# Performance work log

Measured on AMD Instinct MI355X. Metric: run time of the kernel, lower is better.

The kernel has to match this reference:

```python
import jax, jax.numpy as jnp
from jax import lax
import numpy as np

N_ATOMS, N_BONDS, N_GRAPHS = 8192, 32768, 256
EMBED, HIDDEN, DEPTH = 32, 256, 10
ATOM_VOCAB, BOND_VOCAB = 200, 10


def setup_inputs() -> dict:
    key = jax.random.key(0)
    ks = jax.random.split(key, 16)
    f = lambda k, *sh: jax.random.normal(k, sh, dtype=jnp.float32) * 0.05
    return {
        "atom_features": jax.random.randint(ks[0], (N_ATOMS,), 0, ATOM_VOCAB),
        "bond_features": jax.random.randint(ks[1], (N_BONDS,), 0, BOND_VOCAB),
        "adjacency_matrix": jax.random.randint(ks[2], (N_ATOMS, N_ATOMS), 0, 2, dtype=jnp.int32),
        "batch_indices": jax.random.randint(ks[3], (N_ATOMS,), 0, N_GRAPHS),
        "atom_emb": f(ks[4], ATOM_VOCAB, EMBED),
        "bond_emb": f(ks[5], BOND_VOCAB, EMBED),
        "msg_W": f(ks[6], DEPTH, HIDDEN, 2 * EMBED),
        "msg_b": f(ks[7], DEPTH, HIDDEN),
        "gru_Wih": f(ks[8], DEPTH, 3 * EMBED, HIDDEN),
        "gru_Whh": f(ks[9], DEPTH, 3 * EMBED, EMBED),
        "gru_bih": f(ks[10], DEPTH, 3 * EMBED),
        "gru_bhh": f(ks[11], DEPTH, 3 * EMBED),
        "pool_W": f(ks[12], HIDDEN, EMBED),
        "pool_b": f(ks[13], HIDDEN),
    }


def _gmpn(atom_emb, bond_emb, msg_W, msg_b, gru_Wih, gru_Whh, gru_bih, gru_bhh,
          pool_W, pool_b, atom_features, bond_features, adjacency_matrix, batch_indices):
    H = atom_emb[atom_features]                       # [N, E]
    A = (adjacency_matrix > 0).astype(H.dtype)        # [N, N] 0/1
    deg = A.sum(axis=1)                               # [N]
    has_nb = deg > 0
    inv_deg = jnp.where(has_nb, 1.0 / jnp.maximum(deg, 1.0), 0.0)[:, None]

    def layer(h, params):
        W, b, wih, whh, b_ih, b_hh = params
        # mean_j Linear([h_i ; h_j]) = W1 h_i + W2 mean_j h_j + b
        neigh_mean = (A @ h) * inv_deg                # [N, E]
        W1, W2 = W[:, :EMBED], W[:, EMBED:]
        msg = h @ W1.T + neigh_mean @ W2.T + b        # [N, HIDDEN]
        msg = jnp.where(has_nb[:, None], msg, 0.0)    # zero message if no neighbors
        # single-step GRU: input=msg, hidden state=h
        gi = msg @ wih.T + b_ih
        gh = h @ whh.T + b_hh
        ir, iz, inn = jnp.split(gi, 3, axis=-1)
        hr, hz, hn = jnp.split(gh, 3, axis=-1)
        r = jax.nn.sigmoid(ir + hr)
        z = jax.nn.sigmoid(iz + hz)
        n = jnp.tanh(inn + r * hn)
        h_new = (1.0 - z) * n + z * h                 # [N, E]
        return h_new, None

    H, _ = lax.scan(layer, H, (msg_W, msg_b, gru_Wih, gru_Whh, gru_bih, gru_bhh))

    # per-graph mean pooling (zeros for empty graphs), then global_pool linear
    seg_sum = jax.ops.segment_sum(H, batch_indices, num_segments=N_GRAPHS)
    cnt = jax.ops.segment_sum(jnp.ones((H.shape[0],), H.dtype), batch_indices, num_segments=N_GRAPHS)
    graph_mean = jnp.where(cnt[:, None] > 0, seg_sum / jnp.maximum(cnt, 1.0)[:, None], 0.0)
    graph_embeddings = graph_mean @ pool_W.T + pool_b  # [G, HIDDEN]

    bond_embeddings = bond_emb[bond_features]          # [B, E]
    return H, bond_embeddings, graph_embeddings


def reference(atom_features, bond_features, adjacency_matrix, batch_indices,
              atom_emb, bond_emb, msg_W, msg_b, gru_Wih, gru_Whh, gru_bih, gru_bhh,
              pool_W, pool_b):
    return _gmpn(atom_emb, bond_emb, msg_W, msg_b, gru_Wih, gru_Whh, gru_bih, gru_bhh,
                 pool_W, pool_b, atom_features, bond_features, adjacency_matrix, batch_indices)
```

## Files before the change

kernel.cpp:

```cpp
#include <hip/hip_runtime.h>
#include <stdint.h>

typedef __bf16 bf16x8 __attribute__((ext_vector_type(8)));
typedef float f32x4 __attribute__((ext_vector_type(4)));

__device__ __forceinline__ float b2f(unsigned short u){
  unsigned int t = ((unsigned int)u) << 16;
  return __builtin_bit_cast(float, t);
}
__device__ __forceinline__ unsigned short f2b(float f){
  unsigned int x = __builtin_bit_cast(unsigned int, f);
  x = x + 0x7FFFu + ((x >> 16) & 1u);
  return (unsigned short)(x >> 16);
}
__device__ __forceinline__ void spread8(unsigned int B, unsigned int w[4]){
  unsigned int m = __umul24(B, 0x8001u);
  w[0] = __umul24(m & 0x00010001u, 0x3F80u);
  w[1] = __umul24(m & 0x00040004u, 0x0FE0u);
  w[2] = __umul24(m & 0x00100010u, 0x03F8u);
  w[3] = __umul24(m & 0x00400040u, 0x00FEu);
}
__device__ __forceinline__ float fsig(float x){ return 1.f/(1.f + __expf(-x)); }
__device__ __forceinline__ float ftanh(float x){ return 1.f - 2.f/(__expf(2.f*x) + 1.f); }

__global__ void k_prep(const void* s_msgW, const void* s_msgb, const void* s_wih,
                       const void* s_whh, const void* s_bih, const void* s_bhh,
                       const void* s_poolW, const void* s_poolb,
                       const unsigned short* __restrict__ aemb_u16,
                       unsigned short* __restrict__ cw,
                       int* __restrict__ deg, float* __restrict__ seg,
                       float* __restrict__ cnt, int* __restrict__ flag){
  int b = blockIdx.x, t = threadIdx.x;
  unsigned int uu = aemb_u16[2*t];
  int e = (int)((uu >> 7) & 0xFF);
  unsigned long long vote = __ballot(e >= 100 && e <= 127);
  int isb = (__popcll(vote) > 32) ? 1 : 0;
  if (b < 1771){
    int id = b*256 + t;
    if (id < 453248){
      const void* src; int off;
      if      (id < 163840){ src = s_msgW;  off = id; }
      else if (id < 166400){ src = s_msgb;  off = id - 163840; }
      else if (id < 412160){ src = s_wih;   off = id - 166400; }
      else if (id < 442880){ src = s_whh;   off = id - 412160; }
      else if (id < 443840){ src = s_bih;   off = id - 442880; }
      else if (id < 444800){ src = s_bhh;   off = id - 443840; }
      else if (id < 452992){ src = s_poolW; off = id - 444800; }
      else                 { src = s_poolb; off = id - 452992; }
      cw[id] = isb ? ((const unsigned short*)src)[off]
                   : f2b(((const float*)src)[off]);
    }
  } else {
    int id2 = (b - 1771)*256 + t;
    if (id2 < 8192){ deg[id2] = 0; seg[id2] = 0.f; }
    if (id2 < 256) cnt[id2] = 0.f;
    if (b == 1771 && t == 0) flag[0] = isb;
  }
}

__global__ void k_pack(const int* __restrict__ adj, unsigned int* __restrict__ mask3,
                       int* __restrict__ deg){
  int tid = blockIdx.x*256 + threadIdx.x;
  int rb  = tid >> 12;
  int rem = tid & 4095;
  int kgg = rem >> 6;
  int L   = rem & 63;
  int lc = L & 15, q = L >> 4;
  int row = rb*16 + lc;
  const int* arow = adj + (size_t)row*8192 + kgg*128 + q*8;
  unsigned int dw = 0; int pc = 0;
  #pragma unroll
  for (int s=0;s<4;s++){
    const int* p = arow + s*32;
    unsigned int b = 0;
    #pragma unroll
    for (int t=0;t<8;t++) b |= (p[t] > 0 ? 1u : 0u) << t;
    dw |= b << (8*s);
    pc += __popc(b);
  }
  mask3[tid] = dw;
  pc += __shfl_xor(pc, 16);
  pc += __shfl_xor(pc, 32);
  if (q == 0) atomicAdd(deg + row, pc);
}

__global__ void k_bond(const int* __restrict__ bft, const void* __restrict__ braw,
                       const int* __restrict__ flag,
                       unsigned short* __restrict__ outB16, float* __restrict__ outB32){
  int id = blockIdx.x*256 + threadIdx.x;
  int e = id >> 5, c = id & 31;
  int idx = bft[e]*32 + c;
  if (flag[0]) outB16[id] = ((const unsigned short*)braw)[idx];
  else         outB32[id] = ((const float*)braw)[idx];
}

__global__ void k_embed(const int* __restrict__ af, const void* __restrict__ araw,
                        const int* __restrict__ flag,
                        float* __restrict__ hf32, uint4* __restrict__ hfrag){
  __shared__ __align__(16) float sh[512];
  int t = threadIdx.x;
  int r = t >> 5, c = t & 31;
  int row = blockIdx.x*16 + r;
  int idx = af[row]*32 + c;
  float f;
  if (flag[0]) f = b2f(((const unsigned short*)araw)[idx]);
  else         f = ((const float*)araw)[idx];
  hf32[row*32 + c] = f;
  sh[r*32 + c] = f;
  __syncthreads();
  if (t < 64){
    int nt = t >> 5, Lq = t & 31;
    int ks32 = blockIdx.x >> 1, half = blockIdx.x & 1;
    int col = nt*16 + (Lq & 15);
    int rbase = (Lq >> 4)*8;
    unsigned int w[4];
    #pragma unroll
    for (int p=0;p<4;p++){
      unsigned int lo = f2b(sh[(rbase + 2*p    )*32 + col]);
      unsigned int hi = f2b(sh[(rbase + 2*p + 1)*32 + col]);
      w[p] = lo | (hi << 16);
    }
    hfrag[(ks32*2 + nt)*64 + half*32 + Lq] = make_uint4(w[0],w[1],w[2],w[3]);
  }
}

__launch_bounds__(512)
__global__ void k_layer(const unsigned int* __restrict__ mask3,
                        const uint4* __restrict__ hfragIn,
                        unsigned int* __restrict__ hfragOut,
                        float* __restrict__ hf32,
                        const int* __restrict__ deg,
                        const unsigned short* __restrict__ msgW,
                        const unsigned short* __restrict__ msgb,
                        const unsigned short* __restrict__ wih,
                        const unsigned short* __restrict__ whh,
                        const unsigned short* __restrict__ bih,
                        const unsigned short* __restrict__ bhh,
                        const int* __restrict__ bidx,
                        float* __restrict__ seg, float* __restrict__ cnt,
                        unsigned short* __restrict__ out16, float* __restrict__ out32,
                        const int* __restrict__ flag, int last)
{
  __shared__ __align__(16) char uni[33792];
  __shared__ __align__(16) unsigned short sA[32][72];
  __shared__ __align__(16) unsigned short smsg[32][264];
  __shared__ int sdeg[32];

  const int t = threadIdx.x;
  const int b = blockIdx.x;
  const int w = t >> 6, L = t & 63;
  const int q = L >> 4, lc = L & 15;
  const int rowbase = b*32;

  const int r0 = t >> 4;
  const int cl = t & 15;
  const int r  = rowbase + r0;
  const int isb = flag[0];
  const int dgr = deg[r];
  const float invr = dgr > 0 ? 1.f/(float)dgr : 0.f;
  float h0 = hf32[r*32 + cl];
  float h1 = hf32[r*32 + 16 + cl];
  sA[r0][cl]    = f2b(h0);
  sA[r0][16+cl] = f2b(h1);
  if (cl == 0) sdeg[r0] = dgr;

  {
    f32x4 a00={0,0,0,0}, a01={0,0,0,0}, a10={0,0,0,0}, a11={0,0,0,0};
    const unsigned int* mp = mask3 + (size_t)b*8192 + w*512 + L;
    const uint4* bp = hfragIn + (size_t)w*4096 + L;
    for (int g=0; g<8; g++){
      unsigned int mw0 = mp[g*64];
      unsigned int mw1 = mp[4096 + g*64];
      #pragma unroll
      for (int s=0; s<4; s++){
        int ks = g*4 + s;
        uint4 u0 = bp[ks*128];
        uint4 u1 = bp[ks*128 + 64];
        union { unsigned int u[4]; bf16x8 v; } A0, A1, B0, B1;
        spread8((mw0 >> (8*s)) & 0xFFu, A0.u);
        spread8((mw1 >> (8*s)) & 0xFFu, A1.u);
        B0.u[0]=u0.x; B0.u[1]=u0.y; B0.u[2]=u0.z; B0.u[3]=u0.w;
        B1.u[0]=u1.x; B1.u[1]=u1.y; B1.u[2]=u1.z; B1.u[3]=u1.w;
        a00 = __builtin_amdgcn_mfma_f32_16x16x32_bf16(A0.v, B0.v, a00, 0,0,0);
        a01 = __builtin_amdgcn_mfma_f32_16x16x32_bf16(A0.v, B1.v, a01, 0,0,0);
        a10 = __builtin_amdgcn_mfma_f32_16x16x32_bf16(A1.v, B0.v, a10, 0,0,0);
        a11 = __builtin_amdgcn_mfma_f32_16x16x32_bf16(A1.v, B1.v, a11, 0,0,0);
      }
    }
    float* sp = (float*)uni + w*1056;
    #pragma unroll
    for (int rg=0; rg<4; rg++){
      int rw = q*4 + rg;
      sp[rw*33 + lc]         = a00[rg];
      sp[rw*33 + 16 + lc]    = a01[rg];
      sp[(16+rw)*33 + lc]    = a10[rg];
      sp[(16+rw)*33 + 16+lc] = a11[rg];
    }
  }
  __syncthreads();
  {
    const float* spf = (const float*)uni;
    float s0 = 0.f, s1 = 0.f;
    #pragma unroll
    for (int ww=0; ww<8; ww++){
      s0 += spf[ww*1056 + r0*33 + cl];
      s1 += spf[ww*1056 + r0*33 + 16 + cl];
    }
    sA[r0][32+cl] = f2b(s0*invr);
    sA[r0][48+cl] = f2b(s1*invr);
  }
  __syncthreads();
  {
    int rt = w & 1, ntb = (w >> 1)*4;
    union { uint4 u; bf16x8 v; } A0, A1;
    A0.u = *(const uint4*)&sA[rt*16 + lc][q*8];
    A1.u = *(const uint4*)&sA[rt*16 + lc][32 + q*8];
    #pragma unroll
    for (int i=0; i<4; i++){
      int nt = ntb + i;
      union { uint4 u; bf16x8 v; } B0, B1;
      B0.u = *(const uint4*)(msgW + (size_t)(nt*16 + lc)*64 + q*8);
      B1.u = *(const uint4*)(msgW + (size_t)(nt*16 + lc)*64 + 32 + q*8);
      f32x4 am = {0,0,0,0};
      am = __builtin_amdgcn_mfma_f32_16x16x32_bf16(A0.v, B0.v, am, 0,0,0);
      am = __builtin_amdgcn_mfma_f32_16x16x32_bf16(A1.v, B1.v, am, 0,0,0);
      float bv = b2f(msgb[nt*16 + lc]);
      #pragma unroll
      for (int rg=0; rg<4; rg++){
        int rw = rt*16 + q*4 + rg;
        float v = am[rg] + bv;
        if (sdeg[rw] == 0) v = 0.f;
        smsg[rw][nt*16 + lc] = f2b(v);
      }
    }
  }
  __syncthreads();
  {
    float* sgi = (float*)uni;
    float* sgh = (float*)(uni + 12800);
    if (w < 6){
      int nt = w;
      f32x4 g0 = {0,0,0,0}, g1 = {0,0,0,0};
      #pragma unroll
      for (int ks=0; ks<8; ks++){
        union { uint4 u; bf16x8 v; } A0, A1, B;
        B.u  = *(const uint4*)(wih + (size_t)(nt*16 + lc)*256 + ks*32 + q*8);
        A0.u = *(const uint4*)&smsg[lc][ks*32 + q*8];
        A1.u = *(const uint4*)&smsg[16 + lc][ks*32 + q*8];
        g0 = __builtin_amdgcn_mfma_f32_16x16x32_bf16(A0.v, B.v, g0, 0,0,0);
        g1 = __builtin_amdgcn_mfma_f32_16x16x32_bf16(A1.v, B.v, g1, 0,0,0);
      }
      #pragma unroll
      for (int rg=0; rg<4; rg++){
        sgi[(q*4+rg)*100      + nt*16 + lc] = g0[rg];
        sgi[(16+q*4+rg)*100   + nt*16 + lc] = g1[rg];
      }
    } else {
      int rt = w - 6;
      union { uint4 u; bf16x8 v; } A;
      A.u = *(const uint4*)&sA[rt*16 + lc][q*8];
      #pragma unroll
      for (int nt=0; nt<6; nt++){
        union { uint4 u; bf16x8 v; } B;
        B.u = *(const uint4*)(whh + (size_t)(nt*16 + lc)*32 + q*8);
        f32x4 hh = {0,0,0,0};
        hh = __builtin_amdgcn_mfma_f32_16x16x32_bf16(A.v, B.v, hh, 0,0,0);
        #pragma unroll
        for (int rg=0; rg<4; rg++)
          sgh[(rt*16 + q*4+rg)*100 + nt*16 + lc] = hh[rg];
      }
    }
  }
  __syncthreads();
  {
    const float* sgi = (const float*)uni;
    const float* sgh = (const float*)(uni + 12800);
    float ir0 = sgi[r0*100 + cl]    + b2f(bih[cl]),    hr0 = sgh[r0*100 + cl]    + b2f(bhh[cl]);
    float iz0 = sgi[r0*100 + 32+cl] + b2f(bih[32+cl]), hz0 = sgh[r0*100 + 32+cl] + b2f(bhh[32+cl]);
    float in0 = sgi[r0*100 + 64+cl] + b2f(bih[64+cl]), hn0 = sgh[r0*100 + 64+cl] + b2f(bhh[64+cl]);
    float ir1 = sgi[r0*100 + 16+cl] + b2f(bih[16+cl]), hr1 = sgh[r0*100 + 16+cl] + b2f(bhh[16+cl]);
    float iz1 = sgi[r0*100 + 48+cl] + b2f(bih[48+cl]), hz1 = sgh[r0*100 + 48+cl] + b2f(bhh[48+cl]);
    float in1 = sgi[r0*100 + 80+cl] + b2f(bih[80+cl]), hn1 = sgh[r0*100 + 80+cl] + b2f(bhh[80+cl]);
    float rr0 = fsig(ir0 + hr0), zz0 = fsig(iz0 + hz0);
    float rr1 = fsig(ir1 + hr1), zz1 = fsig(iz1 + hz1);
    float nn0 = ftanh(in0 + rr0*hn0);
    float nn1 = ftanh(in1 + rr1*hn1);
    h0 = (1.f - zz0)*nn0 + zz0*h0;
    h1 = (1.f - zz1)*nn1 + zz1*h1;
    hf32[r*32 + cl]      = h0;
    hf32[r*32 + 16 + cl] = h1;
    unsigned int m0 = f2b(h0), m1 = f2b(h1);
    unsigned int p0 = (unsigned int)__shfl_xor((int)m0, 16);
    unsigned int p1 = (unsigned int)__shfl_xor((int)m1, 16);
    if ((r & 1) == 0){
      int ks32 = r >> 5;
      int Lf = ((r >> 3) & 3)*16 + cl;
      int pidx = (r & 7) >> 1;
      hfragOut[((ks32*2 + 0)*64 + Lf)*4 + pidx] = m0 | (p0 << 16);
      hfragOut[((ks32*2 + 1)*64 + Lf)*4 + pidx] = m1 | (p1 << 16);
    }
    if (last){
      if (isb){ out16[r*32 + cl] = (unsigned short)m0; out16[r*32 + 16 + cl] = (unsigned short)m1; }
      else    { out32[r*32 + cl] = h0; out32[r*32 + 16 + cl] = h1; }
      int gb = bidx[r];
      atomicAdd(seg + gb*32 + cl, h0);
      atomicAdd(seg + gb*32 + 16 + cl, h1);
      if (cl == 0) atomicAdd(cnt + gb, 1.f);
    }
  }
}

__global__ void k_pool(const float* __restrict__ seg, const float* __restrict__ cnt,
                       const unsigned short* __restrict__ pw, const unsigned short* __restrict__ pb,
                       const int* __restrict__ flag,
                       unsigned short* __restrict__ outG16, float* __restrict__ outG32){
  int g = blockIdx.x, o = threadIdx.x;
  float cv = cnt[g];
  float ic = cv > 0.f ? 1.f/cv : 0.f;
  float s = 0.f;
  #pragma unroll
  for (int c=0;c<32;c++) s += seg[g*32+c]*ic*b2f(pw[o*32+c]);
  s += b2f(pb[o]);
  if (flag[0]) outG16[g*256 + o] = f2b(s);
  else         outG32[g*256 + o] = s;
}

extern "C" void kernel_launch(void* const* d_in, const int* in_sizes, int n_in,
                              void* d_out, int out_size, void* d_ws, size_t ws_size,
                              hipStream_t stream){
  const int* af   = (const int*)d_in[0];
  const int* bft  = (const int*)d_in[1];
  const int* adj  = (const int*)d_in[2];
  const int* bidx = (const int*)d_in[3];

  char* ws = (char*)d_ws;
  unsigned int*   mask3  = (unsigned int*)(ws + 0);
  unsigned int*   hfrag0 = (unsigned int*)(ws + 8388608);
  unsigned int*   hfrag1 = (unsigned int*)(ws + 8912896);
  float*          hf32   = (float*)(ws + 9437184);
  int*            deg    = (int*)(ws + 10485760);
  float*          seg    = (float*)(ws + 10518528);
  float*          cnt    = (float*)(ws + 10551296);
  int*            flag   = (int*)(ws + 10552320);
  unsigned short* cw     = (unsigned short*)(ws + 10552384);

  unsigned short* o16 = (unsigned short*)d_out;
  float*          o32 = (float*)d_out;

  k_prep<<<1803, 256, 0, stream>>>(d_in[6], d_in[7], d_in[8], d_in[9], d_in[10],
                                   d_in[11], d_in[12], d_in[13],
                                   (const unsigned short*)d_in[4],
                                   cw, deg, seg, cnt, flag);
  k_pack<<<8192, 256, 0, stream>>>(adj, mask3, deg);
  k_bond<<<4096, 256, 0, stream>>>(bft, d_in[5], flag, o16 + 262144, o32 + 262144);
  k_embed<<<512, 512, 0, stream>>>(af, d_in[4], flag, hf32, (uint4*)hfrag0);

  for (int d = 0; d < 10; d++){
    const uint4*  hin  = (const uint4*)((d & 1) ? hfrag1 : hfrag0);
    unsigned int* hout = (d & 1) ? hfrag0 : hfrag1;
    k_layer<<<256, 512, 0, stream>>>(mask3, hin, hout, hf32, deg,
                                     cw + (size_t)d*16384,        cw + 163840 + d*256,
                                     cw + 166400 + (size_t)d*24576, cw + 412160 + d*3072,
                                     cw + 442880 + d*96,          cw + 443840 + d*96,
                                     bidx, seg, cnt, o16, o32, flag, (d == 9) ? 1 : 0);
  }
  k_pool<<<256, 256, 0, stream>>>(seg, cnt, cw + 444800, cw + 452992, flag,
                                  o16 + 1310720, o32 + 1310720);
}
```

Before: 532.7 us.

## Halve layer tile to 16 rows, prefetch adjacency fragments, fold bond gather into prep

The per-layer kernel now processes 16 rows per block with 256 threads and 512 blocks, so more CUs are busy than with the previous 256 blocks. Each wave covers a longer K range. Its adjacency-times-h loop is software-pipelined with register double-buffering of the mask and B fragments. The bond embedding gather is merged into the prep kernel to remove one launch. In exchange, the weight loads are repeated across twice as many blocks, register pressure rises from the prefetch buffers, and each block now handles one row tile instead of two, so fragment reuse drops.

```diff
diff --git a/kernel.cpp b/kernel.cpp
--- a/kernel.cpp
+++ b/kernel.cpp
@@ -27,9 +27,11 @@
                        const void* s_whh, const void* s_bih, const void* s_bhh,
                        const void* s_poolW, const void* s_poolb,
                        const unsigned short* __restrict__ aemb_u16,
+                       const int* __restrict__ bft, const void* __restrict__ braw,
                        unsigned short* __restrict__ cw,
                        int* __restrict__ deg, float* __restrict__ seg,
-                       float* __restrict__ cnt, int* __restrict__ flag){
+                       float* __restrict__ cnt, int* __restrict__ flag,
+                       unsigned short* __restrict__ outB16, float* __restrict__ outB32){
   int b = blockIdx.x, t = threadIdx.x;
   unsigned int uu = aemb_u16[2*t];
   int e = (int)((uu >> 7) & 0xFF);
@@ -50,11 +52,17 @@
       cw[id] = isb ? ((const unsigned short*)src)[off]
                    : f2b(((const float*)src)[off]);
     }
-  } else {
+  } else if (b < 1804){
     int id2 = (b - 1771)*256 + t;
     if (id2 < 8192){ deg[id2] = 0; seg[id2] = 0.f; }
     if (id2 < 256) cnt[id2] = 0.f;
     if (b == 1771 && t == 0) flag[0] = isb;
+  } else {
+    int id = (b - 1804)*256 + t;
+    int e2 = id >> 5, c = id & 31;
+    int idx = bft[e2]*32 + c;
+    if (isb) outB16[id] = ((const unsigned short*)braw)[idx];
+    else     outB32[id] = ((const float*)braw)[idx];
   }
 }
 
@@ -84,16 +92,6 @@
   if (q == 0) atomicAdd(deg + row, pc);
 }
 
-__global__ void k_bond(const int* __restrict__ bft, const void* __restrict__ braw,
-                       const int* __restrict__ flag,
-                       unsigned short* __restrict__ outB16, float* __restrict__ outB32){
-  int id = blockIdx.x*256 + threadIdx.x;
-  int e = id >> 5, c = id & 31;
-  int idx = bft[e]*32 + c;
-  if (flag[0]) outB16[id] = ((const unsigned short*)braw)[idx];
-  else         outB32[id] = ((const float*)braw)[idx];
-}
-
 __global__ void k_embed(const int* __restrict__ af, const void* __restrict__ araw,
                         const int* __restrict__ flag,
                         float* __restrict__ hf32, uint4* __restrict__ hfrag){
@@ -124,7 +122,7 @@
   }
 }
 
-__launch_bounds__(512)
+__launch_bounds__(256, 2)
 __global__ void k_layer(const unsigned int* __restrict__ mask3,
                         const uint4* __restrict__ hfragIn,
                         unsigned int* __restrict__ hfragOut,
@@ -141,16 +139,16 @@
                         unsigned short* __restrict__ out16, float* __restrict__ out32,
                         const int* __restrict__ flag, int last)
 {
-  __shared__ __align__(16) char uni[33792];
-  __shared__ __align__(16) unsigned short sA[32][72];
-  __shared__ __align__(16) unsigned short smsg[32][264];
-  __shared__ int sdeg[32];
+  __shared__ __align__(16) float uni[3200];
+  __shared__ __align__(16) unsigned short sA[16][72];
+  __shared__ __align__(16) unsigned short smsg[16][264];
+  __shared__ int sdeg[16];
 
   const int t = threadIdx.x;
   const int b = blockIdx.x;
   const int w = t >> 6, L = t & 63;
   const int q = L >> 4, lc = L & 15;
-  const int rowbase = b*32;
+  const int rowbase = b*16;
 
   const int r0 = t >> 4;
   const int cl = t & 15;
@@ -165,59 +163,65 @@
   if (cl == 0) sdeg[r0] = dgr;
 
   {
-    f32x4 a00={0,0,0,0}, a01={0,0,0,0}, a10={0,0,0,0}, a11={0,0,0,0};
-    const unsigned int* mp = mask3 + (size_t)b*8192 + w*512 + L;
-    const uint4* bp = hfragIn + (size_t)w*4096 + L;
-    for (int g=0; g<8; g++){
-      unsigned int mw0 = mp[g*64];
-      unsigned int mw1 = mp[4096 + g*64];
+    f32x4 a0 = {0,0,0,0}, a1 = {0,0,0,0};
+    const unsigned int* mp = mask3 + (size_t)b*4096 + (size_t)w*1024 + L;
+    const uint4* bp = hfragIn + (size_t)w*8192 + L;
+    unsigned int mw = mp[0];
+    uint4 buf[8];
+    #pragma unroll
+    for (int u=0; u<8; u++) buf[u] = bp[u*64];
+    #pragma unroll
+    for (int g=0; g<16; g++){
+      unsigned int mw_n = 0;
+      uint4 nbuf[8];
+      if (g < 15){
+        mw_n = mp[(g+1)*64];
+        #pragma unroll
+        for (int u=0; u<8; u++) nbuf[u] = bp[(g+1)*512 + u*64];
+      }
       #pragma unroll
       for (int s=0; s<4; s++){
-        int ks = g*4 + s;
-        uint4 u0 = bp[ks*128];
-        uint4 u1 = bp[ks*128 + 64];
-        union { unsigned int u[4]; bf16x8 v; } A0, A1, B0, B1;
-        spread8((mw0 >> (8*s)) & 0xFFu, A0.u);
-        spread8((mw1 >> (8*s)) & 0xFFu, A1.u);
+        union { unsigned int u[4]; bf16x8 v; } A, B0, B1;
+        spread8((mw >> (8*s)) & 0xFFu, A.u);
+        uint4 u0 = buf[s*2], u1 = buf[s*2+1];
         B0.u[0]=u0.x; B0.u[1]=u0.y; B0.u[2]=u0.z; B0.u[3]=u0.w;
         B1.u[0]=u1.x; B1.u[1]=u1.y; B1.u[2]=u1.z; B1.u[3]=u1.w;
-        a00 = __builtin_amdgcn_mfma_f32_16x16x32_bf16(A0.v, B0.v, a00, 0,0,0);
-        a01 = __builtin_amdgcn_mfma_f32_16x16x32_bf16(A0.v, B1.v, a01, 0,0,0);
-        a10 = __builtin_amdgcn_mfma_f32_16x16x32_bf16(A1.v, B0.v, a10, 0,0,0);
-        a11 = __builtin_amdgcn_mfma_f32_16x16x32_bf16(A1.v, B1.v, a11, 0,0,0);
-      }
-    }
-    float* sp = (float*)uni + w*1056;
+        a0 = __builtin_amdgcn_mfma_f32_16x16x32_bf16(A.v, B0.v, a0, 0,0,0);
+        a1 = __builtin_amdgcn_mfma_f32_16x16x32_bf16(A.v, B1.v, a1, 0,0,0);
+      }
+      mw = mw_n;
+      if (g < 15){
+        #pragma unroll
+        for (int u=0; u<8; u++) buf[u] = nbuf[u];
+      }
+    }
+    float* sp = uni + w*528;
     #pragma unroll
     for (int rg=0; rg<4; rg++){
       int rw = q*4 + rg;
-      sp[rw*33 + lc]         = a00[rg];
-      sp[rw*33 + 16 + lc]    = a01[rg];
-      sp[(16+rw)*33 + lc]    = a10[rg];
-      sp[(16+rw)*33 + 16+lc] = a11[rg];
-    }
-  }
-  __syncthreads();
-  {
-    const float* spf = (const float*)uni;
+      sp[rw*33 + lc]      = a0[rg];
+      sp[rw*33 + 16 + lc] = a1[rg];
+    }
+  }
+  __syncthreads();
+  {
     float s0 = 0.f, s1 = 0.f;
     #pragma unroll
-    for (int ww=0; ww<8; ww++){
-      s0 += spf[ww*1056 + r0*33 + cl];
-      s1 += spf[ww*1056 + r0*33 + 16 + cl];
+    for (int ww=0; ww<4; ww++){
+      s0 += uni[ww*528 + r0*33 + cl];
+      s1 += uni[ww*528 + r0*33 + 16 + cl];
     }
     sA[r0][32+cl] = f2b(s0*invr);
     sA[r0][48+cl] = f2b(s1*invr);
   }
   __syncthreads();
   {
-    int rt = w & 1, ntb = (w >> 1)*4;
     union { uint4 u; bf16x8 v; } A0, A1;
-    A0.u = *(const uint4*)&sA[rt*16 + lc][q*8];
-    A1.u = *(const uint4*)&sA[rt*16 + lc][32 + q*8];
+    A0.u = *(const uint4*)&sA[lc][q*8];
+    A1.u = *(const uint4*)&sA[lc][32 + q*8];
     #pragma unroll
     for (int i=0; i<4; i++){
-      int nt = ntb + i;
+      int nt = w*4 + i;
       union { uint4 u; bf16x8 v; } B0, B1;
       B0.u = *(const uint4*)(msgW + (size_t)(nt*16 + lc)*64 + q*8);
       B1.u = *(const uint4*)(msgW + (size_t)(nt*16 + lc)*64 + 32 + q*8);
@@ -227,7 +231,7 @@
       float bv = b2f(msgb[nt*16 + lc]);
       #pragma unroll
       for (int rg=0; rg<4; rg++){
-        int rw = rt*16 + q*4 + rg;
+        int rw = q*4 + rg;
         float v = am[rg] + bv;
         if (sdeg[rw] == 0) v = 0.f;
         smsg[rw][nt*16 + lc] = f2b(v);
@@ -236,29 +240,28 @@
   }
   __syncthreads();
   {
-    float* sgi = (float*)uni;
-    float* sgh = (float*)(uni + 12800);
-    if (w < 6){
-      int nt = w;
+    float* sgi = uni;
+    float* sgh = uni + 1600;
+    if (w < 3){
+      int nt0 = w*2, nt1 = w*2 + 1;
       f32x4 g0 = {0,0,0,0}, g1 = {0,0,0,0};
       #pragma unroll
       for (int ks=0; ks<8; ks++){
-        union { uint4 u; bf16x8 v; } A0, A1, B;
-        B.u  = *(const uint4*)(wih + (size_t)(nt*16 + lc)*256 + ks*32 + q*8);
-        A0.u = *(const uint4*)&smsg[lc][ks*32 + q*8];
-        A1.u = *(const uint4*)&smsg[16 + lc][ks*32 + q*8];
-        g0 = __builtin_amdgcn_mfma_f32_16x16x32_bf16(A0.v, B.v, g0, 0,0,0);
-        g1 = __builtin_amdgcn_mfma_f32_16x16x32_bf16(A1.v, B.v, g1, 0,0,0);
+        union { uint4 u; bf16x8 v; } A, B0, B1;
+        A.u  = *(const uint4*)&smsg[lc][ks*32 + q*8];
+        B0.u = *(const uint4*)(wih + (size_t)(nt0*16 + lc)*256 + ks*32 + q*8);
+        B1.u = *(const uint4*)(wih + (size_t)(nt1*16 + lc)*256 + ks*32 + q*8);
+        g0 = __builtin_amdgcn_mfma_f32_16x16x32_bf16(A.v, B0.v, g0, 0,0,0);
+        g1 = __builtin_amdgcn_mfma_f32_16x16x32_bf16(A.v, B1.v, g1, 0,0,0);
       }
       #pragma unroll
       for (int rg=0; rg<4; rg++){
-        sgi[(q*4+rg)*100      + nt*16 + lc] = g0[rg];
-        sgi[(16+q*4+rg)*100   + nt*16 + lc] = g1[rg];
+        sgi[(q*4+rg)*100 + nt0*16 + lc] = g0[rg];
+        sgi[(q*4+rg)*100 + nt1*16 + lc] = g1[rg];
       }
     } else {
-      int rt = w - 6;
       union { uint4 u; bf16x8 v; } A;
-      A.u = *(const uint4*)&sA[rt*16 + lc][q*8];
+      A.u = *(const uint4*)&sA[lc][q*8];
       #pragma unroll
       for (int nt=0; nt<6; nt++){
         union { uint4 u; bf16x8 v; } B;
@@ -267,14 +270,14 @@
         hh = __builtin_amdgcn_mfma_f32_16x16x32_bf16(A.v, B.v, hh, 0,0,0);
         #pragma unroll
         for (int rg=0; rg<4; rg++)
-          sgh[(rt*16 + q*4+rg)*100 + nt*16 + lc] = hh[rg];
-      }
-    }
-  }
-  __syncthreads();
-  {
-    const float* sgi = (const float*)uni;
-    const float* sgh = (const float*)(uni + 12800);
+          sgh[(q*4+rg)*100 + nt*16 + lc] = hh[rg];
+      }
+    }
+  }
+  __syncthreads();
+  {
+    const float* sgi = uni;
+    const float* sgh = uni + 1600;
     float ir0 = sgi[r0*100 + cl]    + b2f(bih[cl]),    hr0 = sgh[r0*100 + cl]    + b2f(bhh[cl]);
     float iz0 = sgi[r0*100 + 32+cl] + b2f(bih[32+cl]), hz0 = sgh[r0*100 + 32+cl] + b2f(bhh[32+cl]);
     float in0 = sgi[r0*100 + 64+cl] + b2f(bih[64+cl]), hn0 = sgh[r0*100 + 64+cl] + b2f(bhh[64+cl]);
@@ -347,21 +350,22 @@
   unsigned short* o16 = (unsigned short*)d_out;
   float*          o32 = (float*)d_out;
 
-  k_prep<<<1803, 256, 0, stream>>>(d_in[6], d_in[7], d_in[8], d_in[9], d_in[10],
+  k_prep<<<5900, 256, 0, stream>>>(d_in[6], d_in[7], d_in[8], d_in[9], d_in[10],
                                    d_in[11], d_in[12], d_in[13],
                                    (const unsigned short*)d_in[4],
-                                   cw, deg, seg, cnt, flag);
+                                   bft, d_in[5],
+                                   cw, deg, seg, cnt, flag,
+                                   o16 + 262144, o32 + 262144);
   k_pack<<<8192, 256, 0, stream>>>(adj, mask3, deg);
-  k_bond<<<4096, 256, 0, stream>>>(bft, d_in[5], flag, o16 + 262144, o32 + 262144);
   k_embed<<<512, 512, 0, stream>>>(af, d_in[4], flag, hf32, (uint4*)hfrag0);
 
   for (int d = 0; d < 10; d++){
     const uint4*  hin  = (const uint4*)((d & 1) ? hfrag1 : hfrag0);
     unsigned int* hout = (d & 1) ? hfrag0 : hfrag1;
-    k_layer<<<256, 512, 0, stream>>>(mask3, hin, hout, hf32, deg,
-                                     cw + (size_t)d*16384,        cw + 163840 + d*256,
+    k_layer<<<512, 256, 0, stream>>>(mask3, hin, hout, hf32, deg,
+                                     cw + (size_t)d*16384,          cw + 163840 + d*256,
                                      cw + 166400 + (size_t)d*24576, cw + 412160 + d*3072,
-                                     cw + 442880 + d*96,          cw + 443840 + d*96,
+                                     cw + 442880 + d*96,            cw + 443840 + d*96,
                                      bidx, seg, cnt, o16, o32, flag, (d == 9) ? 1 : 0);
   }
   k_pool<<<256, 256, 0, stream>>>(seg, cnt, cw + 444800, cw + 452992, flag,
```

Measured after the change: 581.8 us. 9.2% more time.

## Fuse embed, all GRU layers and pooling into one cooperative persistent kernel

Applied to the files above, without the earlier changes.

Replaces the per-layer kernel launches, the embed kernel and the pool kernel with a single cooperative kernel of 256 blocks that keeps the hidden state in registers and uses a global atomic barrier between layers. The bond gather is folded into the prep kernel. This removes launch overhead and the fp32 hidden-state round trip through global memory, at the cost of spin-wait grid barriers and requiring all blocks to be co-resident.

```diff
diff --git a/kernel.cpp b/kernel.cpp
--- a/kernel.cpp
+++ b/kernel.cpp
@@ -23,13 +23,28 @@
 __device__ __forceinline__ float fsig(float x){ return 1.f/(1.f + __expf(-x)); }
 __device__ __forceinline__ float ftanh(float x){ return 1.f - 2.f/(__expf(2.f*x) + 1.f); }
 
+__device__ __forceinline__ void gbar(int* bar, int target){
+  __syncthreads();
+  if (threadIdx.x == 0){
+    __threadfence();
+    __hip_atomic_fetch_add(bar, 1, __ATOMIC_RELAXED, __HIP_MEMORY_SCOPE_AGENT);
+    while (__hip_atomic_load(bar, __ATOMIC_RELAXED, __HIP_MEMORY_SCOPE_AGENT) < target)
+      __builtin_amdgcn_s_sleep(1);
+    __threadfence();
+  }
+  __syncthreads();
+}
+
 __global__ void k_prep(const void* s_msgW, const void* s_msgb, const void* s_wih,
                        const void* s_whh, const void* s_bih, const void* s_bhh,
                        const void* s_poolW, const void* s_poolb,
                        const unsigned short* __restrict__ aemb_u16,
+                       const int* __restrict__ bft, const void* __restrict__ braw,
                        unsigned short* __restrict__ cw,
                        int* __restrict__ deg, float* __restrict__ seg,
-                       float* __restrict__ cnt, int* __restrict__ flag){
+                       float* __restrict__ cnt, int* __restrict__ flag,
+                       int* __restrict__ bar,
+                       unsigned short* __restrict__ outB16, float* __restrict__ outB32){
   int b = blockIdx.x, t = threadIdx.x;
   unsigned int uu = aemb_u16[2*t];
   int e = (int)((uu >> 7) & 0xFF);
@@ -50,11 +65,20 @@
       cw[id] = isb ? ((const unsigned short*)src)[off]
                    : f2b(((const float*)src)[off]);
     }
-  } else {
+  } else if (b < 1804){
     int id2 = (b - 1771)*256 + t;
     if (id2 < 8192){ deg[id2] = 0; seg[id2] = 0.f; }
     if (id2 < 256) cnt[id2] = 0.f;
-    if (b == 1771 && t == 0) flag[0] = isb;
+    if (b == 1771){
+      if (t < 16) bar[t] = 0;
+      if (t == 0) flag[0] = isb;
+    }
+  } else {
+    int id = (b - 1804)*256 + t;
+    int e2 = id >> 5, c = id & 31;
+    int idx = bft[e2]*32 + c;
+    if (isb) outB16[id] = ((const unsigned short*)braw)[idx];
+    else     outB32[id] = ((const float*)braw)[idx];
   }
 }
 
@@ -84,245 +108,215 @@
   if (q == 0) atomicAdd(deg + row, pc);
 }
 
-__global__ void k_bond(const int* __restrict__ bft, const void* __restrict__ braw,
-                       const int* __restrict__ flag,
-                       unsigned short* __restrict__ outB16, float* __restrict__ outB32){
-  int id = blockIdx.x*256 + threadIdx.x;
-  int e = id >> 5, c = id & 31;
-  int idx = bft[e]*32 + c;
-  if (flag[0]) outB16[id] = ((const unsigned short*)braw)[idx];
-  else         outB32[id] = ((const float*)braw)[idx];
-}
-
-__global__ void k_embed(const int* __restrict__ af, const void* __restrict__ araw,
-                        const int* __restrict__ flag,
-                        float* __restrict__ hf32, uint4* __restrict__ hfrag){
-  __shared__ __align__(16) float sh[512];
-  int t = threadIdx.x;
-  int r = t >> 5, c = t & 31;
-  int row = blockIdx.x*16 + r;
-  int idx = af[row]*32 + c;
-  float f;
-  if (flag[0]) f = b2f(((const unsigned short*)araw)[idx]);
-  else         f = ((const float*)araw)[idx];
-  hf32[row*32 + c] = f;
-  sh[r*32 + c] = f;
-  __syncthreads();
-  if (t < 64){
-    int nt = t >> 5, Lq = t & 31;
-    int ks32 = blockIdx.x >> 1, half = blockIdx.x & 1;
-    int col = nt*16 + (Lq & 15);
-    int rbase = (Lq >> 4)*8;
-    unsigned int w[4];
-    #pragma unroll
-    for (int p=0;p<4;p++){
-      unsigned int lo = f2b(sh[(rbase + 2*p    )*32 + col]);
-      unsigned int hi = f2b(sh[(rbase + 2*p + 1)*32 + col]);
-      w[p] = lo | (hi << 16);
-    }
-    hfrag[(ks32*2 + nt)*64 + half*32 + Lq] = make_uint4(w[0],w[1],w[2],w[3]);
-  }
-}
-
-__launch_bounds__(512)
-__global__ void k_layer(const unsigned int* __restrict__ mask3,
-                        const uint4* __restrict__ hfragIn,
-                        unsigned int* __restrict__ hfragOut,
-                        float* __restrict__ hf32,
-                        const int* __restrict__ deg,
-                        const unsigned short* __restrict__ msgW,
-                        const unsigned short* __restrict__ msgb,
-                        const unsigned short* __restrict__ wih,
-                        const unsigned short* __restrict__ whh,
-                        const unsigned short* __restrict__ bih,
-                        const unsigned short* __restrict__ bhh,
-                        const int* __restrict__ bidx,
-                        float* __restrict__ seg, float* __restrict__ cnt,
-                        unsigned short* __restrict__ out16, float* __restrict__ out32,
-                        const int* __restrict__ flag, int last)
+__launch_bounds__(512, 1)
+__global__ void k_net(const int* __restrict__ af, const int* __restrict__ bidx,
+                      const void* __restrict__ aemb_raw, const int* __restrict__ flag,
+                      const unsigned int* __restrict__ mask3,
+                      unsigned int* __restrict__ hfrag0, unsigned int* __restrict__ hfrag1,
+                      const int* __restrict__ deg, const unsigned short* __restrict__ cw,
+                      unsigned short* __restrict__ out16, float* __restrict__ out32,
+                      float* __restrict__ seg, float* __restrict__ cnt, int* bar)
 {
-  __shared__ __align__(16) char uni[33792];
+  __shared__ __align__(16) float uni[8448];
   __shared__ __align__(16) unsigned short sA[32][72];
   __shared__ __align__(16) unsigned short smsg[32][264];
   __shared__ int sdeg[32];
 
-  const int t = threadIdx.x;
-  const int b = blockIdx.x;
+  const int t = threadIdx.x, b = blockIdx.x;
   const int w = t >> 6, L = t & 63;
   const int q = L >> 4, lc = L & 15;
-  const int rowbase = b*32;
-
   const int r0 = t >> 4;
   const int cl = t & 15;
-  const int r  = rowbase + r0;
+  const int r  = b*32 + r0;
   const int isb = flag[0];
   const int dgr = deg[r];
   const float invr = dgr > 0 ? 1.f/(float)dgr : 0.f;
-  float h0 = hf32[r*32 + cl];
-  float h1 = hf32[r*32 + 16 + cl];
-  sA[r0][cl]    = f2b(h0);
-  sA[r0][16+cl] = f2b(h1);
+  const int gb = bidx[r];
   if (cl == 0) sdeg[r0] = dgr;
 
+  float h0, h1;
   {
-    f32x4 a00={0,0,0,0}, a01={0,0,0,0}, a10={0,0,0,0}, a11={0,0,0,0};
-    const unsigned int* mp = mask3 + (size_t)b*8192 + w*512 + L;
-    const uint4* bp = hfragIn + (size_t)w*4096 + L;
-    for (int g=0; g<8; g++){
-      unsigned int mw0 = mp[g*64];
-      unsigned int mw1 = mp[4096 + g*64];
-      #pragma unroll
-      for (int s=0; s<4; s++){
-        int ks = g*4 + s;
-        uint4 u0 = bp[ks*128];
-        uint4 u1 = bp[ks*128 + 64];
-        union { unsigned int u[4]; bf16x8 v; } A0, A1, B0, B1;
-        spread8((mw0 >> (8*s)) & 0xFFu, A0.u);
-        spread8((mw1 >> (8*s)) & 0xFFu, A1.u);
-        B0.u[0]=u0.x; B0.u[1]=u0.y; B0.u[2]=u0.z; B0.u[3]=u0.w;
-        B1.u[0]=u1.x; B1.u[1]=u1.y; B1.u[2]=u1.z; B1.u[3]=u1.w;
-        a00 = __builtin_amdgcn_mfma_f32_16x16x32_bf16(A0.v, B0.v, a00, 0,0,0);
-        a01 = __builtin_amdgcn_mfma_f32_16x16x32_bf16(A0.v, B1.v, a01, 0,0,0);
-        a10 = __builtin_amdgcn_mfma_f32_16x16x32_bf16(A1.v, B0.v, a10, 0,0,0);
-        a11 = __builtin_amdgcn_mfma_f32_16x16x32_bf16(A1.v, B1.v, a11, 0,0,0);
-      }
-    }
-    float* sp = (float*)uni + w*1056;
-    #pragma unroll
-    for (int rg=0; rg<4; rg++){
-      int rw = q*4 + rg;
-      sp[rw*33 + lc]         = a00[rg];
-      sp[rw*33 + 16 + lc]    = a01[rg];
-      sp[(16+rw)*33 + lc]    = a10[rg];
-      sp[(16+rw)*33 + 16+lc] = a11[rg];
-    }
-  }
-  __syncthreads();
-  {
-    const float* spf = (const float*)uni;
-    float s0 = 0.f, s1 = 0.f;
-    #pragma unroll
-    for (int ww=0; ww<8; ww++){
-      s0 += spf[ww*1056 + r0*33 + cl];
-      s1 += spf[ww*1056 + r0*33 + 16 + cl];
-    }
-    sA[r0][32+cl] = f2b(s0*invr);
-    sA[r0][48+cl] = f2b(s1*invr);
-  }
-  __syncthreads();
-  {
-    int rt = w & 1, ntb = (w >> 1)*4;
-    union { uint4 u; bf16x8 v; } A0, A1;
-    A0.u = *(const uint4*)&sA[rt*16 + lc][q*8];
-    A1.u = *(const uint4*)&sA[rt*16 + lc][32 + q*8];
-    #pragma unroll
-    for (int i=0; i<4; i++){
-      int nt = ntb + i;
-      union { uint4 u; bf16x8 v; } B0, B1;
-      B0.u = *(const uint4*)(msgW + (size_t)(nt*16 + lc)*64 + q*8);
-      B1.u = *(const uint4*)(msgW + (size_t)(nt*16 + lc)*64 + 32 + q*8);
-      f32x4 am = {0,0,0,0};
-      am = __builtin_amdgcn_mfma_f32_16x16x32_bf16(A0.v, B0.v, am, 0,0,0);
-      am = __builtin_amdgcn_mfma_f32_16x16x32_bf16(A1.v, B1.v, am, 0,0,0);
-      float bv = b2f(msgb[nt*16 + lc]);
-      #pragma unroll
-      for (int rg=0; rg<4; rg++){
-        int rw = rt*16 + q*4 + rg;
-        float v = am[rg] + bv;
-        if (sdeg[rw] == 0) v = 0.f;
-        smsg[rw][nt*16 + lc] = f2b(v);
-      }
-    }
-  }
-  __syncthreads();
-  {
-    float* sgi = (float*)uni;
-    float* sgh = (float*)(uni + 12800);
-    if (w < 6){
-      int nt = w;
-      f32x4 g0 = {0,0,0,0}, g1 = {0,0,0,0};
-      #pragma unroll
-      for (int ks=0; ks<8; ks++){
-        union { uint4 u; bf16x8 v; } A0, A1, B;
-        B.u  = *(const uint4*)(wih + (size_t)(nt*16 + lc)*256 + ks*32 + q*8);
-        A0.u = *(const uint4*)&smsg[lc][ks*32 + q*8];
-        A1.u = *(const uint4*)&smsg[16 + lc][ks*32 + q*8];
-        g0 = __builtin_amdgcn_mfma_f32_16x16x32_bf16(A0.v, B.v, g0, 0,0,0);
-        g1 = __builtin_amdgcn_mfma_f32_16x16x32_bf16(A1.v, B.v, g1, 0,0,0);
-      }
-      #pragma unroll
-      for (int rg=0; rg<4; rg++){
-        sgi[(q*4+rg)*100      + nt*16 + lc] = g0[rg];
-        sgi[(16+q*4+rg)*100   + nt*16 + lc] = g1[rg];
-      }
-    } else {
-      int rt = w - 6;
-      union { uint4 u; bf16x8 v; } A;
-      A.u = *(const uint4*)&sA[rt*16 + lc][q*8];
-      #pragma unroll
-      for (int nt=0; nt<6; nt++){
-        union { uint4 u; bf16x8 v; } B;
-        B.u = *(const uint4*)(whh + (size_t)(nt*16 + lc)*32 + q*8);
-        f32x4 hh = {0,0,0,0};
-        hh = __builtin_amdgcn_mfma_f32_16x16x32_bf16(A.v, B.v, hh, 0,0,0);
-        #pragma unroll
-        for (int rg=0; rg<4; rg++)
-          sgh[(rt*16 + q*4+rg)*100 + nt*16 + lc] = hh[rg];
-      }
-    }
-  }
-  __syncthreads();
-  {
-    const float* sgi = (const float*)uni;
-    const float* sgh = (const float*)(uni + 12800);
-    float ir0 = sgi[r0*100 + cl]    + b2f(bih[cl]),    hr0 = sgh[r0*100 + cl]    + b2f(bhh[cl]);
-    float iz0 = sgi[r0*100 + 32+cl] + b2f(bih[32+cl]), hz0 = sgh[r0*100 + 32+cl] + b2f(bhh[32+cl]);
-    float in0 = sgi[r0*100 + 64+cl] + b2f(bih[64+cl]), hn0 = sgh[r0*100 + 64+cl] + b2f(bhh[64+cl]);
-    float ir1 = sgi[r0*100 + 16+cl] + b2f(bih[16+cl]), hr1 = sgh[r0*100 + 16+cl] + b2f(bhh[16+cl]);
-    float iz1 = sgi[r0*100 + 48+cl] + b2f(bih[48+cl]), hz1 = sgh[r0*100 + 48+cl] + b2f(bhh[48+cl]);
-    float in1 = sgi[r0*100 + 80+cl] + b2f(bih[80+cl]), hn1 = sgh[r0*100 + 80+cl] + b2f(bhh[80+cl]);
-    float rr0 = fsig(ir0 + hr0), zz0 = fsig(iz0 + hz0);
-    float rr1 = fsig(ir1 + hr1), zz1 = fsig(iz1 + hz1);
-    float nn0 = ftanh(in0 + rr0*hn0);
-    float nn1 = ftanh(in1 + rr1*hn1);
-    h0 = (1.f - zz0)*nn0 + zz0*h0;
-    h1 = (1.f - zz1)*nn1 + zz1*h1;
-    hf32[r*32 + cl]      = h0;
-    hf32[r*32 + 16 + cl] = h1;
+    int ai = af[r]*32;
+    if (isb){ const unsigned short* p = (const unsigned short*)aemb_raw;
+              h0 = b2f(p[ai+cl]); h1 = b2f(p[ai+16+cl]); }
+    else    { const float* p = (const float*)aemb_raw;
+              h0 = p[ai+cl]; h1 = p[ai+16+cl]; }
     unsigned int m0 = f2b(h0), m1 = f2b(h1);
+    sA[r0][cl] = (unsigned short)m0; sA[r0][16+cl] = (unsigned short)m1;
     unsigned int p0 = (unsigned int)__shfl_xor((int)m0, 16);
     unsigned int p1 = (unsigned int)__shfl_xor((int)m1, 16);
     if ((r & 1) == 0){
-      int ks32 = r >> 5;
-      int Lf = ((r >> 3) & 3)*16 + cl;
-      int pidx = (r & 7) >> 1;
-      hfragOut[((ks32*2 + 0)*64 + Lf)*4 + pidx] = m0 | (p0 << 16);
-      hfragOut[((ks32*2 + 1)*64 + Lf)*4 + pidx] = m1 | (p1 << 16);
-    }
-    if (last){
-      if (isb){ out16[r*32 + cl] = (unsigned short)m0; out16[r*32 + 16 + cl] = (unsigned short)m1; }
-      else    { out32[r*32 + cl] = h0; out32[r*32 + 16 + cl] = h1; }
-      int gb = bidx[r];
-      atomicAdd(seg + gb*32 + cl, h0);
-      atomicAdd(seg + gb*32 + 16 + cl, h1);
-      if (cl == 0) atomicAdd(cnt + gb, 1.f);
-    }
-  }
-}
-
-__global__ void k_pool(const float* __restrict__ seg, const float* __restrict__ cnt,
-                       const unsigned short* __restrict__ pw, const unsigned short* __restrict__ pb,
-                       const int* __restrict__ flag,
-                       unsigned short* __restrict__ outG16, float* __restrict__ outG32){
-  int g = blockIdx.x, o = threadIdx.x;
-  float cv = cnt[g];
-  float ic = cv > 0.f ? 1.f/cv : 0.f;
-  float s = 0.f;
-  #pragma unroll
-  for (int c=0;c<32;c++) s += seg[g*32+c]*ic*b2f(pw[o*32+c]);
-  s += b2f(pb[o]);
-  if (flag[0]) outG16[g*256 + o] = f2b(s);
-  else         outG32[g*256 + o] = s;
+      int ks32 = r >> 5, Lf = ((r >> 3) & 3)*16 + cl, pidx = (r & 7) >> 1;
+      hfrag0[((ks32*2 + 0)*64 + Lf)*4 + pidx] = m0 | (p0 << 16);
+      hfrag0[((ks32*2 + 1)*64 + Lf)*4 + pidx] = m1 | (p1 << 16);
+    }
+  }
+  gbar(bar + 0, 256);
+
+  for (int d = 0; d < 10; d++){
+    const unsigned int* hfi = (d & 1) ? hfrag1 : hfrag0;
+    unsigned int*       hfo = (d & 1) ? hfrag0 : hfrag1;
+    const unsigned short* msgW = cw + (size_t)d*16384;
+    const unsigned short* msgb = cw + 163840 + d*256;
+    const unsigned short* wih  = cw + 166400 + (size_t)d*24576;
+    const unsigned short* whh  = cw + 412160 + d*3072;
+    const unsigned short* bih  = cw + 442880 + d*96;
+    const unsigned short* bhh  = cw + 443840 + d*96;
+
+    {
+      f32x4 a00={0,0,0,0}, a01={0,0,0,0}, a10={0,0,0,0}, a11={0,0,0,0};
+      const unsigned int* mp = mask3 + (size_t)b*8192 + w*512 + L;
+      const uint4* bp = (const uint4*)hfi + (size_t)w*4096 + L;
+      for (int g=0; g<8; g++){
+        unsigned int mw0 = mp[g*64];
+        unsigned int mw1 = mp[4096 + g*64];
+        #pragma unroll
+        for (int s=0; s<4; s++){
+          int ks = g*4 + s;
+          uint4 u0 = bp[ks*128];
+          uint4 u1 = bp[ks*128 + 64];
+          union { unsigned int u[4]; bf16x8 v; } A0, A1, B0, B1;
+          spread8((mw0 >> (8*s)) & 0xFFu, A0.u);
+          spread8((mw1 >> (8*s)) & 0xFFu, A1.u);
+          B0.u[0]=u0.x; B0.u[1]=u0.y; B0.u[2]=u0.z; B0.u[3]=u0.w;
+          B1.u[0]=u1.x; B1.u[1]=u1.y; B1.u[2]=u1.z; B1.u[3]=u1.w;
+          a00 = __builtin_amdgcn_mfma_f32_16x16x32_bf16(A0.v, B0.v, a00, 0,0,0);
+          a01 = __builtin_amdgcn_mfma_f32_16x16x32_bf16(A0.v, B1.v, a01, 0,0,0);
+          a10 = __builtin_amdgcn_mfma_f32_16x16x32_bf16(A1.v, B0.v, a10, 0,0,0);
+          a11 = __builtin_amdgcn_mfma_f32_16x16x32_bf16(A1.v, B1.v, a11, 0,0,0);
+        }
+      }
+      float* sp = uni + w*1056;
+      #pragma unroll
+      for (int rg=0; rg<4; rg++){
+        int rw = q*4 + rg;
+        sp[rw*33 + lc]         = a00[rg];
+        sp[rw*33 + 16 + lc]    = a01[rg];
+        sp[(16+rw)*33 + lc]    = a10[rg];
+        sp[(16+rw)*33 + 16+lc] = a11[rg];
+      }
+    }
+    __syncthreads();
+    {
+      float s0 = 0.f, s1 = 0.f;
+      #pragma unroll
+      for (int ww=0; ww<8; ww++){
+        s0 += uni[ww*1056 + r0*33 + cl];
+        s1 += uni[ww*1056 + r0*33 + 16 + cl];
+      }
+      sA[r0][32+cl] = f2b(s0*invr);
+      sA[r0][48+cl] = f2b(s1*invr);
+    }
+    __syncthreads();
+    {
+      int rt = w & 1, ntb = (w >> 1)*4;
+      union { uint4 u; bf16x8 v; } A0, A1;
+      A0.u = *(const uint4*)&sA[rt*16 + lc][q*8];
+      A1.u = *(const uint4*)&sA[rt*16 + lc][32 + q*8];
+      #pragma unroll
+      for (int i=0; i<4; i++){
+        int nt = ntb + i;
+        union { uint4 u; bf16x8 v; } B0, B1;
+        B0.u = *(const uint4*)(msgW + (size_t)(nt*16 + lc)*64 + q*8);
+        B1.u = *(const uint4*)(msgW + (size_t)(nt*16 + lc)*64 + 32 + q*8);
+        f32x4 am = {0,0,0,0};
+        am = __builtin_amdgcn_mfma_f32_16x16x32_bf16(A0.v, B0.v, am, 0,0,0);
+        am = __builtin_amdgcn_mfma_f32_16x16x32_bf16(A1.v, B1.v, am, 0,0,0);
+        float bv = b2f(msgb[nt*16 + lc]);
+        #pragma unroll
+        for (int rg=0; rg<4; rg++){
+          int rw = rt*16 + q*4 + rg;
+          float v = am[rg] + bv;
+          if (sdeg[rw] == 0) v = 0.f;
+          smsg[rw][nt*16 + lc] = f2b(v);
+        }
+      }
+    }
+    __syncthreads();
+    {
+      float* sgi = uni;
+      float* sgh = uni + 3200;
+      if (w < 6){
+        int nt = w;
+        f32x4 g0 = {0,0,0,0}, g1 = {0,0,0,0};
+        #pragma unroll
+        for (int ks=0; ks<8; ks++){
+          union { uint4 u; bf16x8 v; } A0, A1, B;
+          B.u  = *(const uint4*)(wih + (size_t)(nt*16 + lc)*256 + ks*32 + q*8);
+          A0.u = *(const uint4*)&smsg[lc][ks*32 + q*8];
+          A1.u = *(const uint4*)&smsg[16 + lc][ks*32 + q*8];
+          g0 = __builtin_amdgcn_mfma_f32_16x16x32_bf16(A0.v, B.v, g0, 0,0,0);
+          g1 = __builtin_amdgcn_mfma_f32_16x16x32_bf16(A1.v, B.v, g1, 0,0,0);
+        }
+        #pragma unroll
+        for (int rg=0; rg<4; rg++){
+          sgi[(q*4+rg)*100    + nt*16 + lc] = g0[rg];
+          sgi[(16+q*4+rg)*100 + nt*16 + lc] = g1[rg];
+        }
+      } else {
+        int rt = w - 6;
+        union { uint4 u; bf16x8 v; } A;
+        A.u = *(const uint4*)&sA[rt*16 + lc][q*8];
+        #pragma unroll
+        for (int nt=0; nt<6; nt++){
+          union { uint4 u; bf16x8 v; } B;
+          B.u = *(const uint4*)(whh + (size_t)(nt*16 + lc)*32 + q*8);
+          f32x4 hh = {0,0,0,0};
+          hh = __builtin_amdgcn_mfma_f32_16x16x32_bf16(A.v, B.v, hh, 0,0,0);
+          #pragma unroll
+          for (int rg=0; rg<4; rg++)
+            sgh[(rt*16 + q*4+rg)*100 + nt*16 + lc] = hh[rg];
+        }
+      }
+    }
+    __syncthreads();
+    {
+      const float* sgi = uni;
+      const float* sgh = uni + 3200;
+      float ir0 = sgi[r0*100 + cl]    + b2f(bih[cl]),    hr0 = sgh[r0*100 + cl]    + b2f(bhh[cl]);
+      float iz0 = sgi[r0*100 + 32+cl] + b2f(bih[32+cl]), hz0 = sgh[r0*100 + 32+cl] + b2f(bhh[32+cl]);
+      float in0 = sgi[r0*100 + 64+cl] + b2f(bih[64+cl]), hn0 = sgh[r0*100 + 64+cl] + b2f(bhh[64+cl]);
+      float ir1 = sgi[r0*100 + 16+cl] + b2f(bih[16+cl]), hr1 = sgh[r0*100 + 16+cl] + b2f(bhh[16+cl]);
+      float iz1 = sgi[r0*100 + 48+cl] + b2f(bih[48+cl]), hz1 = sgh[r0*100 + 48+cl] + b2f(bhh[48+cl]);
+      float in1 = sgi[r0*100 + 80+cl] + b2f(bih[80+cl]), hn1 = sgh[r0*100 + 80+cl] + b2f(bhh[80+cl]);
+      float rr0 = fsig(ir0 + hr0), zz0 = fsig(iz0 + hz0);
+      float rr1 = fsig(ir1 + hr1), zz1 = fsig(iz1 + hz1);
+      float nn0 = ftanh(in0 + rr0*hn0);
+      float nn1 = ftanh(in1 + rr1*hn1);
+      h0 = (1.f - zz0)*nn0 + zz0*h0;
+      h1 = (1.f - zz1)*nn1 + zz1*h1;
+      unsigned int m0 = f2b(h0), m1 = f2b(h1);
+      sA[r0][cl] = (unsigned short)m0; sA[r0][16+cl] = (unsigned short)m1;
+      unsigned int p0 = (unsigned int)__shfl_xor((int)m0, 16);
+      unsigned int p1 = (unsigned int)__shfl_xor((int)m1, 16);
+      if ((r & 1) == 0){
+        int ks32 = r >> 5, Lf = ((r >> 3) & 3)*16 + cl, pidx = (r & 7) >> 1;
+        hfo[((ks32*2 + 0)*64 + Lf)*4 + pidx] = m0 | (p0 << 16);
+        hfo[((ks32*2 + 1)*64 + Lf)*4 + pidx] = m1 | (p1 << 16);
+      }
+      if (d == 9){
+        if (isb){ out16[r*32 + cl] = (unsigned short)m0; out16[r*32 + 16 + cl] = (unsigned short)m1; }
+        else    { out32[r*32 + cl] = h0; out32[r*32 + 16 + cl] = h1; }
+        atomicAdd(seg + gb*32 + cl, h0);
+        atomicAdd(seg + gb*32 + 16 + cl, h1);
+        if (cl == 0) atomicAdd(cnt + gb, 1.f);
+      }
+    }
+    gbar(bar + 1 + d, 256);
+  }
+
+  if (t < 256){
+    const unsigned short* pw = cw + 444800;
+    const unsigned short* pb = cw + 452992;
+    float cv = cnt[b];
+    float ic = cv > 0.f ? 1.f/cv : 0.f;
+    float s = 0.f;
+    #pragma unroll
+    for (int c=0;c<32;c++) s += seg[b*32+c]*ic*b2f(pw[t*32+c]);
+    s += b2f(pb[t]);
+    if (isb) out16[1310720 + b*256 + t] = f2b(s);
+    else     out32[1310720 + b*256 + t] = s;
+  }
 }
 
 extern "C" void kernel_launch(void* const* d_in, const int* in_sizes, int n_in,
@@ -337,33 +331,32 @@
   unsigned int*   mask3  = (unsigned int*)(ws + 0);
   unsigned int*   hfrag0 = (unsigned int*)(ws + 8388608);
   unsigned int*   hfrag1 = (unsigned int*)(ws + 8912896);
-  float*          hf32   = (float*)(ws + 9437184);
-  int*            deg    = (int*)(ws + 10485760);
-  float*          seg    = (float*)(ws + 10518528);
-  float*          cnt    = (float*)(ws + 10551296);
-  int*            flag   = (int*)(ws + 10552320);
-  unsigned short* cw     = (unsigned short*)(ws + 10552384);
+  int*            deg    = (int*)(ws + 9437184);
+  float*          seg    = (float*)(ws + 9469952);
+  float*          cnt    = (float*)(ws + 9502720);
+  int*            flag   = (int*)(ws + 9503744);
+  int*            bar    = (int*)(ws + 9503808);
+  unsigned short* cw     = (unsigned short*)(ws + 9503872);
 
   unsigned short* o16 = (unsigned short*)d_out;
   float*          o32 = (float*)d_out;
 
-  k_prep<<<1803, 256, 0, stream>>>(d_in[6], d_in[7], d_in[8], d_in[9], d_in[10],
+  k_prep<<<5900, 256, 0, stream>>>(d_in[6], d_in[7], d_in[8], d_in[9], d_in[10],
                                    d_in[11], d_in[12], d_in[13],
                                    (const unsigned short*)d_in[4],
-                                   cw, deg, seg, cnt, flag);
+                                   bft, d_in[5],
+                                   cw, deg, seg, cnt, flag, bar,
+                                   o16 + 262144, o32 + 262144);
   k_pack<<<8192, 256, 0, stream>>>(adj, mask3, deg);
-  k_bond<<<4096, 256, 0, stream>>>(bft, d_in[5], flag, o16 + 262144, o32 + 262144);
-  k_embed<<<512, 512, 0, stream>>>(af, d_in[4], flag, hf32, (uint4*)hfrag0);
-
-  for (int d = 0; d < 10; d++){
-    const uint4*  hin  = (const uint4*)((d & 1) ? hfrag1 : hfrag0);
-    unsigned int* hout = (d & 1) ? hfrag0 : hfrag1;
-    k_layer<<<256, 512, 0, stream>>>(mask3, hin, hout, hf32, deg,
-                                     cw + (size_t)d*16384,        cw + 163840 + d*256,
-                                     cw + 166400 + (size_t)d*24576, cw + 412160 + d*3072,
-                                     cw + 442880 + d*96,          cw + 443840 + d*96,
-                                     bidx, seg, cnt, o16, o32, flag, (d == 9) ? 1 : 0);
-  }
-  k_pool<<<256, 256, 0, stream>>>(seg, cnt, cw + 444800, cw + 452992, flag,
-                                  o16 + 1310720, o32 + 1310720);
-}
+
+  const void* aemb = d_in[4];
+  const unsigned int* mask3c = mask3;
+  const int* degc = deg;
+  const unsigned short* cwc = cw;
+  const int* flagc = flag;
+  void* ka[] = { (void*)&af, (void*)&bidx, (void*)&aemb, (void*)&flagc,
+                 (void*)&mask3c, (void*)&hfrag0, (void*)&hfrag1, (void*)&degc,
+                 (void*)&cwc, (void*)&o16, (void*)&o32, (void*)&seg, (void*)&cnt,
+                 (void*)&bar };
+  hipLaunchCooperativeKernel((void*)k_net, dim3(256), dim3(512), ka, 0, stream);
+}
```

New measurement: 765.4 us. 1.44x slower.
